# Kernel optimization log

Hardware: AMD Instinct MI355X
Metric: run time of the kernel (lower is better)

## Reference

```python
import jax, jax.numpy as jnp
import numpy as np


def setup_inputs() -> dict:
    key = jax.random.key(0)
    ks = jax.random.split(key, 7)
    B, T, E, H = 4, 4096, 1024, 64
    return {
        "idx": jax.random.normal(ks[0], (B, T, E), dtype=jnp.float32),
        "Wq": jax.random.normal(ks[1], (E, H), dtype=jnp.float32) * (E ** -0.5),
        "bq": jax.random.normal(ks[2], (H,), dtype=jnp.float32) * 0.01,
        "Wk": jax.random.normal(ks[3], (E, H), dtype=jnp.float32) * (E ** -0.5),
        "bk": jax.random.normal(ks[4], (H,), dtype=jnp.float32) * 0.01,
        "Wv": jax.random.normal(ks[5], (E, H), dtype=jnp.float32) * (E ** -0.5),
        "bv": jax.random.normal(ks[6], (H,), dtype=jnp.float32) * 0.01,
    }


def reference(idx, Wq, bq, Wk, bk, Wv, bv):
    # idx: [B, T, E]
    d = idx.shape[-1]  # note: torch code scales by n_embd**-0.5, NOT head_size
    Q = idx @ Wq + bq  # [B, T, H]
    K = idx @ Wk + bk
    V = idx @ Wv + bv
    # scores; NOTE: original torch code calls wei.masked_fill(...) non-in-place
    # and discards the result, so no causal mask is applied. No softmax either.
    wei = jnp.einsum("bth,bsh->bts", Q, K) * (d ** -0.5)  # [B, T, T]
    out = jnp.einsum("bts,bsh->bth", wei, V)  # [B, T, H]
    return out
```

## Files before the change

kernel.cpp:

```cpp
#include <hip/hip_runtime.h>


typedef __attribute__((ext_vector_type(8))) short bf16x8;
typedef __attribute__((ext_vector_type(4))) float f32x4;

#define MFMA16(a, b, c) __builtin_amdgcn_mfma_f32_16x16x32_bf16((a), (b), (c), 0, 0, 0)

__device__ __forceinline__ unsigned short f2bf(float f) {
    unsigned int u = __float_as_uint(f);
    u += 0x7fffu + ((u >> 16) & 1u);
    return (unsigned short)(u >> 16);
}

__global__ void prep(const float* __restrict__ Wq, const float* __restrict__ Wk,
                     const float* __restrict__ Wv, unsigned short* __restrict__ WB) {
    int t = blockIdx.x * 256 + threadIdx.x;
    int k0i = t / 768;
    int rem = t - k0i * 768;
    int nt = rem >> 6, lane = rem & 63;
    int n = nt * 16 + (lane & 15);
    int kb = k0i * 32 + ((lane >> 4) * 8);
    int mm = n >> 6, h = n & 63;
    const float* W = (mm == 0) ? Wq : (mm == 1) ? Wk : Wv;
    float sc = (mm == 1) ? 0.03125f : 1.0f;
    bf16x8 v;
    #pragma unroll
    for (int j = 0; j < 8; j++) v[j] = (short)f2bf(W[(size_t)(kb + j) * 64 + h] * sc);
    *(bf16x8*)(WB + (size_t)t * 8) = v;
}

__global__ __launch_bounds__(256, 3) void qkv(
    const float* __restrict__ idx, const unsigned short* __restrict__ WB,
    const float* __restrict__ bq, const float* __restrict__ bk, const float* __restrict__ bv,
    unsigned short* __restrict__ Q, unsigned short* __restrict__ Kt,
    unsigned short* __restrict__ Vt) {
    __shared__ float red[2][64][49];
    const int lane = threadIdx.x & 63, kh = threadIdx.x >> 6;
    const int r0 = blockIdx.x * 16;

    const float* aP = idx + (size_t)(r0 + (lane & 15)) * 1024 + kh * 256 + ((lane >> 4) * 8);

    float4 af[16];
    #pragma unroll
    for (int it = 0; it < 8; it++) {
        af[it * 2]     = *(const float4*)(aP + it * 32);
        af[it * 2 + 1] = *(const float4*)(aP + it * 32 + 4);
    }
    bf16x8 aF[8];
    #pragma unroll
    for (int it = 0; it < 8; it++) {
        float4 lo = af[it * 2], hi = af[it * 2 + 1];
        bf16x8 a;
        a[0] = (short)f2bf(lo.x); a[1] = (short)f2bf(lo.y);
        a[2] = (short)f2bf(lo.z); a[3] = (short)f2bf(lo.w);
        a[4] = (short)f2bf(hi.x); a[5] = (short)f2bf(hi.y);
        a[6] = (short)f2bf(hi.z); a[7] = (short)f2bf(hi.w);
        aF[it] = a;
    }

    const f32x4 z4 = {0.f, 0.f, 0.f, 0.f};
    f32x4 acc[12];
    #pragma unroll
    for (int i = 0; i < 12; i++) acc[i] = z4;

    #pragma unroll
    for (int i = 0; i < 8; i++) {
        const unsigned short* Bp = WB + (size_t)(((kh * 8 + i) * 12) * 64 + lane) * 8;
        #pragma unroll
        for (int nt = 0; nt < 12; nt++) {
            bf16x8 bb = *(const bf16x8*)(Bp + nt * 512);
            acc[nt] = MFMA16(aF[i], bb, acc[nt]);
        }
    }

    if (kh >= 2) {
        #pragma unroll
        for (int nt = 0; nt < 12; nt++)
            #pragma unroll
            for (int reg = 0; reg < 4; reg++)
                red[kh - 2][lane][nt * 4 + reg] = acc[nt][reg];
    }
    __syncthreads();
    if (kh < 2) {
        #pragma unroll
        for (int nt = 0; nt < 12; nt++)
            #pragma unroll
            for (int reg = 0; reg < 4; reg++)
                acc[nt][reg] += red[kh][lane][nt * 4 + reg];
    }
    __syncthreads();
    if (kh == 1) {
        #pragma unroll
        for (int nt = 0; nt < 12; nt++)
            #pragma unroll
            for (int reg = 0; reg < 4; reg++)
                red[0][lane][nt * 4 + reg] = acc[nt][reg];
    }
    __syncthreads();
    if (kh == 0) {
        #pragma unroll
        for (int nt = 0; nt < 12; nt++) {
            int m = nt >> 2;
            int h = (nt & 3) * 16 + (lane & 15);
            float bias = (m == 0) ? bq[h] : (m == 1) ? bk[h] * 0.03125f : bv[h];
            int rbase = r0 + (lane >> 4) * 4;
            #pragma unroll
            for (int reg = 0; reg < 4; reg++) {
                float s = acc[nt][reg] + red[0][lane][nt * 4 + reg] + bias;
                int r = rbase + reg;
                unsigned short v = f2bf(s);
                if (m == 0) {
                    Q[(size_t)r * 64 + h] = v;
                } else {
                    int b = r >> 12, t = r & 4095;
                    unsigned short* dst = (m == 1) ? Kt : Vt;
                    dst[(size_t)b * 262144 + h * 4096 + t] = v;
                }
            }
        }
    }
}

__global__ __launch_bounds__(256) void ktv_partial(
    const unsigned short* __restrict__ Kt, const unsigned short* __restrict__ Vt,
    float* __restrict__ part) {
    const int lane = threadIdx.x & 63, wave = threadIdx.x >> 6;
    const int c = blockIdx.x, b = blockIdx.y;
    const unsigned short* Kb = Kt + (size_t)b * 262144;
    const unsigned short* Vb = Vt + (size_t)b * 262144;
    const f32x4 z4 = {0.f, 0.f, 0.f, 0.f};
    f32x4 acc[4] = {z4, z4, z4, z4};
    const int m  = 16 * wave + (lane & 15);
    const int tq = (lane >> 4) * 8;
    #pragma unroll
    for (int it = 0; it < 4; it++) {
        int t0 = c * 128 + it * 32 + tq;
        bf16x8 a = *(const bf16x8*)&Kb[(size_t)m * 4096 + t0];
        #pragma unroll
        for (int nt = 0; nt < 4; nt++) {
            bf16x8 bb = *(const bf16x8*)&Vb[(size_t)(nt * 16 + (lane & 15)) * 4096 + t0];
            acc[nt] = MFMA16(a, bb, acc[nt]);
        }
    }
    float* P = part + (size_t)(b * 32 + c) * 4096;
    const int rowb = 16 * wave + (lane >> 4) * 4;
    #pragma unroll
    for (int nt = 0; nt < 4; nt++)
        #pragma unroll
        for (int reg = 0; reg < 4; reg++)
            P[(rowb + reg) * 64 + nt * 16 + (lane & 15)] = acc[nt][reg];
}

__global__ void reduce_m(const float* __restrict__ part,
                         unsigned short* __restrict__ Mt) {
    int i = blockIdx.x * 256 + threadIdx.x;
    int b = i >> 12, h1 = (i >> 6) & 63, h2 = i & 63;
    float s = 0.f;
    #pragma unroll
    for (int cc = 0; cc < 32; cc++)
        s += part[(size_t)(b * 32 + cc) * 4096 + h1 * 64 + h2];
    Mt[(size_t)b * 4096 + h2 * 64 + h1] = f2bf(s);
}

__global__ __launch_bounds__(256) void qm(
    const unsigned short* __restrict__ Q, const unsigned short* __restrict__ Mt,
    float* __restrict__ out) {
    const int lane = threadIdx.x & 63, wave = threadIdx.x >> 6;
    const int r0 = blockIdx.x * 64;
    const int b  = r0 >> 12;
    const f32x4 z4 = {0.f, 0.f, 0.f, 0.f};
    f32x4 acc[4] = {z4, z4, z4, z4};
    const int rr = r0 + 16 * wave + (lane & 15);
    const int kq = (lane >> 4) * 8;
    #pragma unroll
    for (int ks = 0; ks < 2; ks++) {
        int k0 = ks * 32;
        bf16x8 a = *(const bf16x8*)&Q[(size_t)rr * 64 + k0 + kq];
        #pragma unroll
        for (int nt = 0; nt < 4; nt++) {
            bf16x8 bb = *(const bf16x8*)&Mt[(size_t)b * 4096 + (nt * 16 + (lane & 15)) * 64 + k0 + kq];
            acc[nt] = MFMA16(a, bb, acc[nt]);
        }
    }
    const int rowb = r0 + 16 * wave + (lane >> 4) * 4;
    #pragma unroll
    for (int nt = 0; nt < 4; nt++)
        #pragma unroll
        for (int reg = 0; reg < 4; reg++)
            out[(size_t)(rowb + reg) * 64 + nt * 16 + (lane & 15)] = acc[nt][reg];
}

extern "C" void kernel_launch(void* const* d_in, const int* in_sizes, int n_in,
                              void* d_out, int out_size, void* d_ws, size_t ws_size,
                              hipStream_t stream) {
    const float* idx = (const float*)d_in[0];
    const float* Wq  = (const float*)d_in[1];
    const float* bq  = (const float*)d_in[2];
    const float* Wk  = (const float*)d_in[3];
    const float* bk  = (const float*)d_in[4];
    const float* Wv  = (const float*)d_in[5];
    const float* bv  = (const float*)d_in[6];
    float* out = (float*)d_out;

    char* ws = (char*)d_ws;
    unsigned short* WB = (unsigned short*)(ws);
    float*          Pp = (float*)(ws);
    unsigned short* Q  = (unsigned short*)(ws + (2048u << 10));
    unsigned short* Kt = (unsigned short*)(ws + (4096u << 10));
    unsigned short* Vt = (unsigned short*)(ws + (6144u << 10));
    unsigned short* Mt = (unsigned short*)(ws + (8192u << 10));

    hipLaunchKernelGGL(prep,        dim3(96),     dim3(256), 0, stream, Wq, Wk, Wv, WB);
    hipLaunchKernelGGL(qkv,         dim3(1024),   dim3(256), 0, stream,
                       idx, WB, bq, bk, bv, Q, Kt, Vt);
    hipLaunchKernelGGL(ktv_partial, dim3(32, 4),  dim3(256), 0, stream, Kt, Vt, Pp);
    hipLaunchKernelGGL(reduce_m,    dim3(64),     dim3(256), 0, stream, Pp, Mt);
    hipLaunchKernelGGL(qm,          dim3(256),    dim3(256), 0, stream, Q, Mt, out);
}
```

Measured before the change: 138.2 us.

## Restructure QKV projection to split N across waves with double-buffered LDS loads

```diff
diff --git a/kernel.cpp b/kernel.cpp
--- a/kernel.cpp
+++ b/kernel.cpp
@@ -10,6 +10,12 @@
     unsigned int u = __float_as_uint(f);
     u += 0x7fffu + ((u >> 16) & 1u);
     return (unsigned short)(u >> 16);
+}
+
+__device__ __forceinline__ void load_lds16(const float* g, float* l) {
+    __builtin_amdgcn_global_load_lds(
+        (const __attribute__((address_space(1))) unsigned int*)g,
+        (__attribute__((address_space(3))) unsigned int*)l, 16, 0, 0);
 }
 
 __global__ void prep(const float* __restrict__ Wq, const float* __restrict__ Wk,
@@ -29,91 +35,78 @@
     *(bf16x8*)(WB + (size_t)t * 8) = v;
 }
 
-__global__ __launch_bounds__(256, 3) void qkv(
+__global__ __launch_bounds__(256, 2) void qkv(
     const float* __restrict__ idx, const unsigned short* __restrict__ WB,
     const float* __restrict__ bq, const float* __restrict__ bk, const float* __restrict__ bv,
     unsigned short* __restrict__ Q, unsigned short* __restrict__ Kt,
     unsigned short* __restrict__ Vt) {
-    __shared__ float red[2][64][49];
-    const int lane = threadIdx.x & 63, kh = threadIdx.x >> 6;
-    const int r0 = blockIdx.x * 16;
-
-    const float* aP = idx + (size_t)(r0 + (lane & 15)) * 1024 + kh * 256 + ((lane >> 4) * 8);
-
-    float4 af[16];
-    #pragma unroll
-    for (int it = 0; it < 8; it++) {
-        af[it * 2]     = *(const float4*)(aP + it * 32);
-        af[it * 2 + 1] = *(const float4*)(aP + it * 32 + 4);
-    }
-    bf16x8 aF[8];
-    #pragma unroll
-    for (int it = 0; it < 8; it++) {
-        float4 lo = af[it * 2], hi = af[it * 2 + 1];
-        bf16x8 a;
-        a[0] = (short)f2bf(lo.x); a[1] = (short)f2bf(lo.y);
-        a[2] = (short)f2bf(lo.z); a[3] = (short)f2bf(lo.w);
-        a[4] = (short)f2bf(hi.x); a[5] = (short)f2bf(hi.y);
-        a[6] = (short)f2bf(hi.z); a[7] = (short)f2bf(hi.w);
-        aF[it] = a;
-    }
+    __shared__ float As[2][32][260];
+    const int lane = threadIdx.x & 63, w = threadIdx.x >> 6;
+    const int r0 = blockIdx.x * 32;
+
+    auto stage_load = [&](int s, int buf) {
+        #pragma unroll
+        for (int i = 0; i < 8; i++) {
+            int r = i * 4 + w;
+            const float* g = idx + (size_t)(r0 + r) * 1024 + s * 256 + lane * 4;
+            load_lds16(g, &As[buf][r][0]);
+        }
+    };
 
     const f32x4 z4 = {0.f, 0.f, 0.f, 0.f};
-    f32x4 acc[12];
-    #pragma unroll
-    for (int i = 0; i < 12; i++) acc[i] = z4;
-
-    #pragma unroll
-    for (int i = 0; i < 8; i++) {
-        const unsigned short* Bp = WB + (size_t)(((kh * 8 + i) * 12) * 64 + lane) * 8;
-        #pragma unroll
-        for (int nt = 0; nt < 12; nt++) {
-            bf16x8 bb = *(const bf16x8*)(Bp + nt * 512);
-            acc[nt] = MFMA16(aF[i], bb, acc[nt]);
-        }
-    }
-
-    if (kh >= 2) {
-        #pragma unroll
-        for (int nt = 0; nt < 12; nt++)
+    f32x4 acc[2][3];
+    #pragma unroll
+    for (int mt = 0; mt < 2; mt++)
+        #pragma unroll
+        for (int j = 0; j < 3; j++) acc[mt][j] = z4;
+
+    stage_load(0, 0);
+    for (int s = 0; s < 4; s++) {
+        __syncthreads();
+        if (s < 3) stage_load(s + 1, (s + 1) & 1);
+        const int buf = s & 1;
+        #pragma unroll
+        for (int kk = 0; kk < 8; kk++) {
+            bf16x8 aF[2];
             #pragma unroll
-            for (int reg = 0; reg < 4; reg++)
-                red[kh - 2][lane][nt * 4 + reg] = acc[nt][reg];
-    }
-    __syncthreads();
-    if (kh < 2) {
-        #pragma unroll
-        for (int nt = 0; nt < 12; nt++)
+            for (int mt = 0; mt < 2; mt++) {
+                const float* ap = &As[buf][mt * 16 + (lane & 15)][kk * 32 + (lane >> 4) * 8];
+                float4 lo = *(const float4*)ap;
+                float4 hi = *(const float4*)(ap + 4);
+                bf16x8 a;
+                a[0] = (short)f2bf(lo.x); a[1] = (short)f2bf(lo.y);
+                a[2] = (short)f2bf(lo.z); a[3] = (short)f2bf(lo.w);
+                a[4] = (short)f2bf(hi.x); a[5] = (short)f2bf(hi.y);
+                a[6] = (short)f2bf(hi.z); a[7] = (short)f2bf(hi.w);
+                aF[mt] = a;
+            }
+            const unsigned short* Bp = WB + (size_t)(((s * 8 + kk) * 12) * 64 + lane) * 8;
             #pragma unroll
-            for (int reg = 0; reg < 4; reg++)
-                acc[nt][reg] += red[kh][lane][nt * 4 + reg];
-    }
-    __syncthreads();
-    if (kh == 1) {
-        #pragma unroll
-        for (int nt = 0; nt < 12; nt++)
-            #pragma unroll
-            for (int reg = 0; reg < 4; reg++)
-                red[0][lane][nt * 4 + reg] = acc[nt][reg];
-    }
-    __syncthreads();
-    if (kh == 0) {
-        #pragma unroll
-        for (int nt = 0; nt < 12; nt++) {
-            int m = nt >> 2;
-            int h = (nt & 3) * 16 + (lane & 15);
-            float bias = (m == 0) ? bq[h] : (m == 1) ? bk[h] * 0.03125f : bv[h];
-            int rbase = r0 + (lane >> 4) * 4;
+            for (int j = 0; j < 3; j++) {
+                int nt = w + j * 4;
+                bf16x8 bb = *(const bf16x8*)(Bp + nt * 512);
+                acc[0][j] = MFMA16(aF[0], bb, acc[0][j]);
+                acc[1][j] = MFMA16(aF[1], bb, acc[1][j]);
+            }
+        }
+    }
+
+    const int h = w * 16 + (lane & 15);
+    #pragma unroll
+    for (int j = 0; j < 3; j++) {
+        float bias = (j == 0) ? bq[h] : (j == 1) ? bk[h] * 0.03125f : bv[h];
+        #pragma unroll
+        for (int mt = 0; mt < 2; mt++) {
+            int rbase = r0 + mt * 16 + (lane >> 4) * 4;
             #pragma unroll
             for (int reg = 0; reg < 4; reg++) {
-                float s = acc[nt][reg] + red[0][lane][nt * 4 + reg] + bias;
                 int r = rbase + reg;
-                unsigned short v = f2bf(s);
-                if (m == 0) {
+                unsigned short v = f2bf(acc[mt][j][reg] + bias);
+                if (j == 0) {
                     Q[(size_t)r * 64 + h] = v;
                 } else {
                     int b = r >> 12, t = r & 4095;
-                    unsigned short* dst = (m == 1) ? Kt : Vt;
+                    unsigned short* dst = (j == 1) ? Kt : Vt;
                     dst[(size_t)b * 262144 + h * 4096 + t] = v;
                 }
             }
@@ -211,7 +204,7 @@
     unsigned short* Mt = (unsigned short*)(ws + (8192u << 10));
 
     hipLaunchKernelGGL(prep,        dim3(96),     dim3(256), 0, stream, Wq, Wk, Wv, WB);
-    hipLaunchKernelGGL(qkv,         dim3(1024),   dim3(256), 0, stream,
+    hipLaunchKernelGGL(qkv,         dim3(512),    dim3(256), 0, stream,
                        idx, WB, bq, bk, bv, Q, Kt, Vt);
     hipLaunchKernelGGL(ktv_partial, dim3(32, 4),  dim3(256), 0, stream, Kt, Vt, Pp);
     hipLaunchKernelGGL(reduce_m,    dim3(64),     dim3(256), 0, stream, Pp, Mt);
```

Result: faster. 129.7 us (-6.1%).
